# Kernel optimization log

Measured on AMD Instinct MI355X. Metric: run time of the kernel, lower is better.

## Reference

```python
import jax, jax.numpy as jnp
import numpy as np
jax.config.update("jax_enable_x64", True)

N_NODES = 1_000_000
N_ELEM = 2_000_000


def setup_inputs() -> dict:
    key = jax.random.key(0)
    ks = jax.random.split(key, 12)
    f32 = jnp.float32
    return {
        "pred_raw": jax.random.normal(ks[0], (N_NODES, 3), f32),
        "F_ext": jax.random.normal(ks[1], (N_NODES, 3), f32),
        "connectivity": jax.random.randint(ks[2], (N_ELEM, 2), 0, N_NODES, dtype=jnp.int64),
        "elem_lengths": jax.random.uniform(ks[3], (N_ELEM,), f32) + f32(0.5),  # keep L away from 0
        "prop_E": jax.random.uniform(ks[4], (N_ELEM,), f32),
        "prop_A": jax.random.uniform(ks[5], (N_ELEM,), f32),
        "prop_I22": jax.random.uniform(ks[6], (N_ELEM,), f32),
        "elem_directions": jax.random.normal(ks[7], (N_ELEM, 3), f32),
        "ux_c": jax.random.uniform(ks[8], (1,), f32) + f32(0.5),
        "uz_c": jax.random.uniform(ks[9], (1,), f32) + f32(0.5),
        "theta_c": jax.random.uniform(ks[10], (1,), f32) + f32(0.5),
        "F_c": jax.random.uniform(ks[11], (1,), f32) + f32(0.5),
    }


def reference(pred_raw, F_ext, connectivity, elem_lengths, prop_E, prop_A,
              prop_I22, elem_directions, ux_c, uz_c, theta_c, F_c):
    axial_weight = 1.0
    f64 = jnp.float64
    p = pred_raw.astype(f64)
    # physical displacements (scalar characteristic scales; single-graph branch)
    u_phys = jnp.stack([
        p[:, 0] * ux_c.astype(f64)[0],
        p[:, 1] * uz_c.astype(f64)[0],
        p[:, 2] * theta_c.astype(f64)[0],
    ], axis=1)  # [N, 3]

    nA = connectivity[:, 0]
    nB = connectivity[:, 1]
    L = elem_lengths.astype(f64)
    EA = (prop_E * prop_A).astype(f64)
    EI = (prop_E * prop_I22).astype(f64)
    c = elem_directions[:, 0].astype(f64)
    s = elem_directions[:, 2].astype(f64)

    uA = u_phys[nA]  # [E, 3] gather
    uB = u_phys[nB]
    u_A = c * uA[:, 0] + s * uA[:, 1]
    w_A = -s * uA[:, 0] + c * uA[:, 1]
    t_A = -uA[:, 2]
    u_B = c * uB[:, 0] + s * uB[:, 1]
    w_B = -s * uB[:, 0] + c * uB[:, 1]
    t_B = -uB[:, 2]

    ea_l = EA / L
    ei_l = EI / L
    ei_l2 = EI / L ** 2
    ei_l3 = EI / L ** 3

    # analytic expansion of d^T K_loc d (same math as the batched 6x6 bmm)
    du = u_A - u_B
    dw = w_A - w_B
    tsum = t_A + t_B
    q = (axial_weight * ea_l * du ** 2
         + 12.0 * ei_l3 * dw ** 2
         + 12.0 * ei_l2 * dw * tsum
         + 4.0 * ei_l * (t_A ** 2 + t_B ** 2 + t_A * t_B))
    U = 0.5 * jnp.sum(q)

    W = jnp.sum(F_ext.astype(f64) * u_phys)
    Pi = U - W

    E_c = jnp.maximum((F_c * ux_c).astype(f64)[0], 1e-30)  # n_graphs = 1
    Pi_norm = Pi / E_c
    return Pi_norm.astype(jnp.float32), u_phys.astype(jnp.float32)
```

## Files before the change

### kernel.cpp

```cpp
#include <hip/hip_runtime.h>


#define NBLOCKS 2048
#define NTHREADS 256

__device__ __forceinline__ double elem_energy(
    double L, double EA, double EI, double c, double s,
    double uA0, double uA1, double uA2,
    double uB0, double uB1, double uB2)
{
    const double u_A =  c*uA0 + s*uA1;
    const double w_A = -s*uA0 + c*uA1;
    const double t_A = -uA2;
    const double u_B =  c*uB0 + s*uB1;
    const double w_B = -s*uB0 + c*uB1;
    const double t_B = -uB2;

    const double du = u_A - u_B, dw = w_A - w_B, ts = t_A + t_B;
    const double invL = 1.0 / L;
    const double ea_l  = EA * invL;
    const double ei_l  = EI * invL;
    const double ei_l2 = ei_l * invL;
    const double ei_l3 = ei_l2 * invL;
    return ea_l * du * du
         + 12.0 * ei_l3 * dw * dw
         + 12.0 * ei_l2 * dw * ts
         + 4.0  * ei_l  * (t_A*t_A + t_B*t_B + t_A*t_B);
}

__global__ __launch_bounds__(NTHREADS) void fused_kernel(
    const float* __restrict__ pred,
    const float* __restrict__ Fext,
    const int*   __restrict__ conn,
    const float* __restrict__ Lf,
    const float* __restrict__ Ef,
    const float* __restrict__ Af,
    const float* __restrict__ I22f,
    const float* __restrict__ dirs,
    const float* __restrict__ ux_c,
    const float* __restrict__ uz_c,
    const float* __restrict__ th_c,
    float* __restrict__ u_out,
    double* __restrict__ acc,
    int n_node_vec4,
    int n_elem_pair)
{
    const int T  = gridDim.x * NTHREADS;
    const int t0 = blockIdx.x * NTHREADS + threadIdx.x;

    const double sx = (double)ux_c[0];
    const double sy = (double)uz_c[0];
    const double sz = (double)th_c[0];

    double w = 0.0;
    double q = 0.0;

    int  i    = t0;
    bool have = (i < n_elem_pair);
    int4   cn = make_int4(0,0,0,0);
    float2 Lv = make_float2(1,1), Ev = make_float2(0,0),
           Av = make_float2(0,0), Iv = make_float2(0,0),
           d0 = make_float2(0,0), d1 = make_float2(0,0), d2 = make_float2(0,0);
    if (have) {
        cn = ((const int4*)conn)[i];
        Lv = ((const float2*)Lf)[i];
        Ev = ((const float2*)Ef)[i];
        Av = ((const float2*)Af)[i];
        Iv = ((const float2*)I22f)[i];
        d0 = ((const float2*)dirs)[3*i + 0];
        d1 = ((const float2*)dirs)[3*i + 1];
        d2 = ((const float2*)dirs)[3*i + 2];
    }

    for (int j = t0; j < n_node_vec4; j += T) {
        const float4 p = ((const float4*)pred)[j];
        const float4 f = ((const float4*)Fext)[j];
        const int m = j % 3;
        const double a = (m == 0) ? sx : (m == 1) ? sy : sz;
        const double b = (m == 0) ? sy : (m == 1) ? sz : sx;
        const double c = (m == 0) ? sz : (m == 1) ? sx : sy;
        const double u0 = (double)p.x * a;
        const double u1 = (double)p.y * b;
        const double u2 = (double)p.z * c;
        const double u3 = (double)p.w * a;
        ((float4*)u_out)[j] = make_float4((float)u0, (float)u1, (float)u2, (float)u3);
        w += (double)f.x * u0 + (double)f.y * u1 + (double)f.z * u2 + (double)f.w * u3;
    }

    while (have) {
        const float pA0x = pred[3*cn.x + 0];
        const float pA0y = pred[3*cn.x + 1];
        const float pA0z = pred[3*cn.x + 2];
        const float pB0x = pred[3*cn.y + 0];
        const float pB0y = pred[3*cn.y + 1];
        const float pB0z = pred[3*cn.y + 2];
        const float pA1x = pred[3*cn.z + 0];
        const float pA1y = pred[3*cn.z + 1];
        const float pA1z = pred[3*cn.z + 2];
        const float pB1x = pred[3*cn.w + 0];
        const float pB1y = pred[3*cn.w + 1];
        const float pB1z = pred[3*cn.w + 2];

        const int  inext = i + T;
        const bool hnext = (inext < n_elem_pair);
        int4   cn2 = cn;
        float2 Lv2 = Lv, Ev2 = Ev, Av2 = Av, Iv2 = Iv, d02 = d0, d12 = d1, d22 = d2;
        if (hnext) {
            cn2 = ((const int4*)conn)[inext];
            Lv2 = ((const float2*)Lf)[inext];
            Ev2 = ((const float2*)Ef)[inext];
            Av2 = ((const float2*)Af)[inext];
            Iv2 = ((const float2*)I22f)[inext];
            d02 = ((const float2*)dirs)[3*inext + 0];
            d12 = ((const float2*)dirs)[3*inext + 1];
            d22 = ((const float2*)dirs)[3*inext + 2];
        }

        q += elem_energy((double)Lv.x,
                         (double)(Ev.x * Av.x),
                         (double)(Ev.x * Iv.x),
                         (double)d0.x, (double)d1.x,
                         (double)pA0x * sx, (double)pA0y * sy, (double)pA0z * sz,
                         (double)pB0x * sx, (double)pB0y * sy, (double)pB0z * sz);
        q += elem_energy((double)Lv.y,
                         (double)(Ev.y * Av.y),
                         (double)(Ev.y * Iv.y),
                         (double)d1.y, (double)d2.y,
                         (double)pA1x * sx, (double)pA1y * sy, (double)pA1z * sz,
                         (double)pB1x * sx, (double)pB1y * sy, (double)pB1z * sz);

        i = inext; have = hnext;
        cn = cn2; Lv = Lv2; Ev = Ev2; Av = Av2; Iv = Iv2; d0 = d02; d1 = d12; d2 = d22;
    }

    __shared__ double smem_w[4];
    __shared__ double smem_q[4];
    const int lane = threadIdx.x & 63;
    const int wave = threadIdx.x >> 6;
    #pragma unroll
    for (int off = 32; off > 0; off >>= 1) {
        w += __shfl_down(w, off, 64);
        q += __shfl_down(q, off, 64);
    }
    if (lane == 0) { smem_w[wave] = w; smem_q[wave] = q; }
    __syncthreads();
    if (threadIdx.x == 0) {
        atomicAdd(acc + 0, smem_q[0] + smem_q[1] + smem_q[2] + smem_q[3]);
        atomicAdd(acc + 1, smem_w[0] + smem_w[1] + smem_w[2] + smem_w[3]);
    }
}

__global__ void finalize_kernel(const double* __restrict__ acc,
                                const float* __restrict__ Fc,
                                const float* __restrict__ ux_c,
                                float* __restrict__ out) {
    const double U  = 0.5 * acc[0];
    const double W  = acc[1];
    const double Ec = fmax((double)(Fc[0] * ux_c[0]), 1e-30);
    out[0] = (float)((U - W) / Ec);
}

extern "C" void kernel_launch(void* const* d_in, const int* in_sizes, int n_in,
                              void* d_out, int out_size, void* d_ws, size_t ws_size,
                              hipStream_t stream) {
    const float* pred  = (const float*)d_in[0];
    const float* Fext  = (const float*)d_in[1];
    const int*   conn  = (const int*)  d_in[2];
    const float* Lf    = (const float*)d_in[3];
    const float* Ef    = (const float*)d_in[4];
    const float* Af    = (const float*)d_in[5];
    const float* I22f  = (const float*)d_in[6];
    const float* dirs  = (const float*)d_in[7];
    const float* ux_c  = (const float*)d_in[8];
    const float* uz_c  = (const float*)d_in[9];
    const float* th_c  = (const float*)d_in[10];
    const float* Fc    = (const float*)d_in[11];

    float*  out = (float*)d_out;
    double* acc = (double*)d_ws;

    const int n_flat      = in_sizes[0];
    const int n_elem      = in_sizes[3];
    const int n_node_vec4 = n_flat / 4;
    const int n_elem_pair = n_elem / 2;

    hipMemsetAsync(d_ws, 0, 2 * sizeof(double), stream);

    fused_kernel<<<NBLOCKS, NTHREADS, 0, stream>>>(
        pred, Fext, conn, Lf, Ef, Af, I22f, dirs, ux_c, uz_c, th_c,
        out + 1, acc, n_node_vec4, n_elem_pair);

    finalize_kernel<<<1, 1, 0, stream>>>(acc, Fc, ux_c, out);
}
```

Measured before the change: 202.4 us.

## Use nontemporal streaming loads, paired-float node gathers, and per-block partial reduction

Switches the streaming element and force arrays and the displacement output to nontemporal loads and stores, so they are less likely to evict the node array that the random gathers read. Each node's three floats are now fetched with two aligned 8-byte loads instead of three scalar loads. The global atomics and the memset are replaced by per-block partial sums that a 256-thread finalize kernel reduces. This drops one launch and the atomic contention, at the cost of a slightly larger final reduction; the finalize loop bound is tied to NBLOCKS.

```diff
diff --git a/kernel.cpp b/kernel.cpp
--- a/kernel.cpp
+++ b/kernel.cpp
@@ -3,6 +3,10 @@
 
 #define NBLOCKS 2048
 #define NTHREADS 256
+
+typedef float v4f __attribute__((ext_vector_type(4)));
+typedef float v2f __attribute__((ext_vector_type(2)));
+typedef int   v4i __attribute__((ext_vector_type(4)));
 
 __device__ __forceinline__ double elem_energy(
     double L, double EA, double EI, double c, double s,
@@ -26,6 +30,19 @@
          + 12.0 * ei_l3 * dw * dw
          + 12.0 * ei_l2 * dw * ts
          + 4.0  * ei_l  * (t_A*t_A + t_B*t_B + t_A*t_B);
+}
+
+__device__ __forceinline__ void gather_node(const float* __restrict__ pred,
+                                            int n, float& x, float& y, float& z)
+{
+    const int base = 3 * n;
+    const int e0   = base & ~1;
+    const v2f a = *(const v2f*)(pred + e0);
+    const v2f b = *(const v2f*)(pred + e0 + 2);
+    const bool odd = (base & 1) != 0;
+    x = odd ? a.y : a.x;
+    y = odd ? b.x : a.y;
+    z = odd ? b.y : b.x;
 }
 
 __global__ __launch_bounds__(NTHREADS) void fused_kernel(
@@ -41,7 +58,7 @@
     const float* __restrict__ uz_c,
     const float* __restrict__ th_c,
     float* __restrict__ u_out,
-    double* __restrict__ acc,
+    double* __restrict__ partial,
     int n_node_vec4,
     int n_elem_pair)
 {
@@ -57,24 +74,23 @@
 
     int  i    = t0;
     bool have = (i < n_elem_pair);
-    int4   cn = make_int4(0,0,0,0);
-    float2 Lv = make_float2(1,1), Ev = make_float2(0,0),
-           Av = make_float2(0,0), Iv = make_float2(0,0),
-           d0 = make_float2(0,0), d1 = make_float2(0,0), d2 = make_float2(0,0);
+    v4i cn = {0,0,0,0};
+    v2f Lv = {1,1}, Ev = {0,0}, Av = {0,0}, Iv = {0,0},
+        d0 = {0,0}, d1 = {0,0}, d2 = {0,0};
     if (have) {
-        cn = ((const int4*)conn)[i];
-        Lv = ((const float2*)Lf)[i];
-        Ev = ((const float2*)Ef)[i];
-        Av = ((const float2*)Af)[i];
-        Iv = ((const float2*)I22f)[i];
-        d0 = ((const float2*)dirs)[3*i + 0];
-        d1 = ((const float2*)dirs)[3*i + 1];
-        d2 = ((const float2*)dirs)[3*i + 2];
+        cn = __builtin_nontemporal_load((const v4i*)conn + i);
+        Lv = __builtin_nontemporal_load((const v2f*)Lf + i);
+        Ev = __builtin_nontemporal_load((const v2f*)Ef + i);
+        Av = __builtin_nontemporal_load((const v2f*)Af + i);
+        Iv = __builtin_nontemporal_load((const v2f*)I22f + i);
+        d0 = __builtin_nontemporal_load((const v2f*)dirs + 3*i + 0);
+        d1 = __builtin_nontemporal_load((const v2f*)dirs + 3*i + 1);
+        d2 = __builtin_nontemporal_load((const v2f*)dirs + 3*i + 2);
     }
 
     for (int j = t0; j < n_node_vec4; j += T) {
-        const float4 p = ((const float4*)pred)[j];
-        const float4 f = ((const float4*)Fext)[j];
+        const v4f p = *((const v4f*)pred + j);
+        const v4f f = __builtin_nontemporal_load((const v4f*)Fext + j);
         const int m = j % 3;
         const double a = (m == 0) ? sx : (m == 1) ? sy : sz;
         const double b = (m == 0) ? sy : (m == 1) ? sz : sx;
@@ -83,37 +99,32 @@
         const double u1 = (double)p.y * b;
         const double u2 = (double)p.z * c;
         const double u3 = (double)p.w * a;
-        ((float4*)u_out)[j] = make_float4((float)u0, (float)u1, (float)u2, (float)u3);
+        v4f o; o.x = (float)u0; o.y = (float)u1; o.z = (float)u2; o.w = (float)u3;
+        __builtin_nontemporal_store(o, (v4f*)u_out + j);
         w += (double)f.x * u0 + (double)f.y * u1 + (double)f.z * u2 + (double)f.w * u3;
     }
 
     while (have) {
-        const float pA0x = pred[3*cn.x + 0];
-        const float pA0y = pred[3*cn.x + 1];
-        const float pA0z = pred[3*cn.x + 2];
-        const float pB0x = pred[3*cn.y + 0];
-        const float pB0y = pred[3*cn.y + 1];
-        const float pB0z = pred[3*cn.y + 2];
-        const float pA1x = pred[3*cn.z + 0];
-        const float pA1y = pred[3*cn.z + 1];
-        const float pA1z = pred[3*cn.z + 2];
-        const float pB1x = pred[3*cn.w + 0];
-        const float pB1y = pred[3*cn.w + 1];
-        const float pB1z = pred[3*cn.w + 2];
+        float pA0x, pA0y, pA0z, pB0x, pB0y, pB0z;
+        float pA1x, pA1y, pA1z, pB1x, pB1y, pB1z;
+        gather_node(pred, cn.x, pA0x, pA0y, pA0z);
+        gather_node(pred, cn.y, pB0x, pB0y, pB0z);
+        gather_node(pred, cn.z, pA1x, pA1y, pA1z);
+        gather_node(pred, cn.w, pB1x, pB1y, pB1z);
 
         const int  inext = i + T;
         const bool hnext = (inext < n_elem_pair);
-        int4   cn2 = cn;
-        float2 Lv2 = Lv, Ev2 = Ev, Av2 = Av, Iv2 = Iv, d02 = d0, d12 = d1, d22 = d2;
+        v4i cn2 = cn;
+        v2f Lv2 = Lv, Ev2 = Ev, Av2 = Av, Iv2 = Iv, d02 = d0, d12 = d1, d22 = d2;
         if (hnext) {
-            cn2 = ((const int4*)conn)[inext];
-            Lv2 = ((const float2*)Lf)[inext];
-            Ev2 = ((const float2*)Ef)[inext];
-            Av2 = ((const float2*)Af)[inext];
-            Iv2 = ((const float2*)I22f)[inext];
-            d02 = ((const float2*)dirs)[3*inext + 0];
-            d12 = ((const float2*)dirs)[3*inext + 1];
-            d22 = ((const float2*)dirs)[3*inext + 2];
+            cn2 = __builtin_nontemporal_load((const v4i*)conn + inext);
+            Lv2 = __builtin_nontemporal_load((const v2f*)Lf + inext);
+            Ev2 = __builtin_nontemporal_load((const v2f*)Ef + inext);
+            Av2 = __builtin_nontemporal_load((const v2f*)Af + inext);
+            Iv2 = __builtin_nontemporal_load((const v2f*)I22f + inext);
+            d02 = __builtin_nontemporal_load((const v2f*)dirs + 3*inext + 0);
+            d12 = __builtin_nontemporal_load((const v2f*)dirs + 3*inext + 1);
+            d22 = __builtin_nontemporal_load((const v2f*)dirs + 3*inext + 2);
         }
 
         q += elem_energy((double)Lv.x,
@@ -145,19 +156,39 @@
     if (lane == 0) { smem_w[wave] = w; smem_q[wave] = q; }
     __syncthreads();
     if (threadIdx.x == 0) {
-        atomicAdd(acc + 0, smem_q[0] + smem_q[1] + smem_q[2] + smem_q[3]);
-        atomicAdd(acc + 1, smem_w[0] + smem_w[1] + smem_w[2] + smem_w[3]);
-    }
-}
-
-__global__ void finalize_kernel(const double* __restrict__ acc,
-                                const float* __restrict__ Fc,
-                                const float* __restrict__ ux_c,
-                                float* __restrict__ out) {
-    const double U  = 0.5 * acc[0];
-    const double W  = acc[1];
-    const double Ec = fmax((double)(Fc[0] * ux_c[0]), 1e-30);
-    out[0] = (float)((U - W) / Ec);
+        partial[2*blockIdx.x + 0] = smem_q[0] + smem_q[1] + smem_q[2] + smem_q[3];
+        partial[2*blockIdx.x + 1] = smem_w[0] + smem_w[1] + smem_w[2] + smem_w[3];
+    }
+}
+
+__global__ __launch_bounds__(256) void finalize_kernel(
+    const double* __restrict__ partial,
+    const float* __restrict__ Fc,
+    const float* __restrict__ ux_c,
+    float* __restrict__ out)
+{
+    __shared__ double smem_q[4];
+    __shared__ double smem_w[4];
+    double q = 0.0, w = 0.0;
+    for (int b = threadIdx.x; b < NBLOCKS; b += 256) {
+        q += partial[2*b + 0];
+        w += partial[2*b + 1];
+    }
+    const int lane = threadIdx.x & 63;
+    const int wave = threadIdx.x >> 6;
+    #pragma unroll
+    for (int off = 32; off > 0; off >>= 1) {
+        q += __shfl_down(q, off, 64);
+        w += __shfl_down(w, off, 64);
+    }
+    if (lane == 0) { smem_q[wave] = q; smem_w[wave] = w; }
+    __syncthreads();
+    if (threadIdx.x == 0) {
+        const double U  = 0.5 * (smem_q[0] + smem_q[1] + smem_q[2] + smem_q[3]);
+        const double W  = smem_w[0] + smem_w[1] + smem_w[2] + smem_w[3];
+        const double Ec = fmax((double)(Fc[0] * ux_c[0]), 1e-30);
+        out[0] = (float)((U - W) / Ec);
+    }
 }
 
 extern "C" void kernel_launch(void* const* d_in, const int* in_sizes, int n_in,
@@ -176,19 +207,17 @@
     const float* th_c  = (const float*)d_in[10];
     const float* Fc    = (const float*)d_in[11];
 
-    float*  out = (float*)d_out;
-    double* acc = (double*)d_ws;
+    float*  out     = (float*)d_out;
+    double* partial = (double*)d_ws;
 
     const int n_flat      = in_sizes[0];
     const int n_elem      = in_sizes[3];
     const int n_node_vec4 = n_flat / 4;
     const int n_elem_pair = n_elem / 2;
 
-    hipMemsetAsync(d_ws, 0, 2 * sizeof(double), stream);
-
     fused_kernel<<<NBLOCKS, NTHREADS, 0, stream>>>(
         pred, Fext, conn, Lf, Ef, Af, I22f, dirs, ux_c, uz_c, th_c,
-        out + 1, acc, n_node_vec4, n_elem_pair);
-
-    finalize_kernel<<<1, 1, 0, stream>>>(acc, Fc, ux_c, out);
-}
+        out + 1, partial, n_node_vec4, n_elem_pair);
+
+    finalize_kernel<<<1, 256, 0, stream>>>(partial, Fc, ux_c, out);
+}
```

Result: faster. 190.1 us (-6.1%).
